# Optimization experiments

Hardware: AMD Instinct MI355X
Metric: run time of the kernel (lower is better)

The kernel has to match this reference:

```python
import jax, jax.numpy as jnp
import numpy as np

K = 11  # masked conv3d kernel size

def mask_A(k):
    # mask type 'A': flattened (i,j,t) positions with current_id < k^3//2 + 1
    # (current_id starts at 1) -> first k^3//2 positions are 1.
    m = (np.arange(k ** 3) < (k ** 3) // 2).astype(np.float32).reshape(k, k, k)
    return jnp.asarray(m)

def conv3d(x, w, b, pad):
    out = jax.lax.conv_general_dilated(
        x, w, window_strides=(1, 1, 1), padding=[(pad, pad)] * 3,
        dimension_numbers=('NCDHW', 'OIDHW', 'NCDHW'))
    return out + b[None, :, None, None, None]

def conv2d(x, w, b, pad):
    out = jax.lax.conv_general_dilated(
        x, w, window_strides=(1, 1), padding=[(pad, pad)] * 2,
        dimension_numbers=('NCHW', 'OIHW', 'NCHW'))
    return out + b[None, :, None, None]

def pconv(x, w, b):
    # 1x1x1 conv3d as channel GEMM; w: [O, C]
    return jnp.einsum('bcdhw,oc->bodhw', x, w) + b[None, :, None, None, None]

def _phi(z):
    return 0.5 * (1.0 + jax.lax.erf(z / jnp.sqrt(2.0).astype(z.dtype)))

def setup_inputs() -> dict:
    key = jax.random.key(0)
    ks = jax.random.split(key, 12)
    M = 192
    B, H, W = 1, 48, 48
    s = 0.02
    x = jax.random.normal(ks[0], (B, M, H, W), jnp.float32)
    hyper = jax.random.normal(ks[1], (B, 2 * M, H, W), jnp.float32)
    W3 = s * jax.random.normal(ks[2], (M, 2 * M, 3, 3), jnp.float32)
    b3 = jnp.zeros((M,), jnp.float32)
    W1 = s * jax.random.normal(ks[3], (24, 1, K, K, K), jnp.float32)
    b1 = jnp.zeros((24,), jnp.float32)
    Wa = s * jax.random.normal(ks[4], (48, 25), jnp.float32)
    ba = jnp.zeros((48,), jnp.float32)
    Wb = s * jax.random.normal(ks[5], (96, 48), jnp.float32)
    bb = jnp.zeros((96,), jnp.float32)
    Wc = s * jax.random.normal(ks[6], (9, 96), jnp.float32)
    bc = jnp.zeros((9,), jnp.float32)
    return {"x": x, "hyper": hyper, "W3": W3, "b3": b3, "W1": W1, "b1": b1,
            "Wa": Wa, "ba": ba, "Wb": Wb, "bb": bb, "Wc": Wc, "bc": bc}

def reference(x, hyper, W3, b3, W1, b1, Wa, ba, Wb, bb, Wc, bc):
    # x: [B,M,H,W], hyper: [B,2M,H,W]
    x5 = x[:, None]                                   # [B,1,M,H,W]
    h = conv2d(hyper, W3, b3, 1)[:, None]             # [B,1,M,H,W]
    W1m = W1 * mask_A(K)[None, None]                  # causal mask re-applied each fwd
    x1 = conv3d(x5, W1m, b1, 5)                       # [B,24,M,H,W]
    t = jnp.concatenate([x1, h], axis=1)              # [B,25,M,H,W]
    t = jax.nn.relu(pconv(t, Wa, ba))                 # [B,48,M,H,W]
    t = jax.nn.relu(pconv(t, Wb, bb))                 # [B,96,M,H,W]
    out = pconv(t, Wc, bc)                            # [B,9,M,H,W]
    # 3-component weighted Gaussian entropy model
    mu = out[:, 0:3]
    sc = out[:, 3:6]
    sc = jnp.abs(jnp.where(sc == 0.0, 1e-9, sc))
    w = jax.nn.softmax(out[:, 6:9], axis=1)
    xe = x[:, None]                                   # [B,1,M,H,W]
    lik = jnp.abs(_phi((xe + 0.5 - mu) / sc) - _phi((xe - 0.5 - mu) / sc))
    p3 = jnp.sum(w * lik, axis=1)                     # [B,M,H,W]
    return (p3, out)
```

## Files before the change

### kernel.cpp

```cpp
#include <hip/hip_runtime.h>
#include <hip/hip_fp16.h>
#include <math.h>

#define HW    2304
#define NPOS  442368

typedef _Float16 f16x8 __attribute__((ext_vector_type(8)));
typedef __fp16   h16x2 __attribute__((ext_vector_type(2)));
typedef float    f32x4 __attribute__((ext_vector_type(4)));

__device__ __forceinline__ float phi_f(float z) {
    return 0.5f * (1.0f + erff(z * 0.70710678118654752f));
}
__device__ __forceinline__ unsigned short f2h(float v) {
    _Float16 h = (_Float16)v;
    return *reinterpret_cast<unsigned short*>(&h);
}
__device__ __forceinline__ unsigned int pk2(float a, float b) {
    return (unsigned int)f2h(a) | ((unsigned int)f2h(b) << 16);
}
__device__ __forceinline__ unsigned int pkrtz(float a, float b) {
    h16x2 h = __builtin_amdgcn_cvt_pkrtz(a, b);
    return *reinterpret_cast<unsigned int*>(&h);
}

__global__ __launch_bounds__(256) void prep_all(const float* __restrict__ hyper,
                                                const float* __restrict__ W3,
                                                const float* __restrict__ W1,
                                                const float* __restrict__ Wa,
                                                const float* __restrict__ ba,
                                                const float* __restrict__ b1,
                                                const float* __restrict__ Wb,
                                                const float* __restrict__ bb,
                                                const float* __restrict__ Wc,
                                                const float* __restrict__ xg,
                                                unsigned short* __restrict__ hyperTp,
                                                unsigned short* __restrict__ apack,
                                                unsigned short* __restrict__ pk,
                                                unsigned short* __restrict__ xhp) {
    const int bx = blockIdx.x;
    if (bx < 948) {
        __shared__ float s[32][33];
        const int pt = bx % 79, it = bx / 79;
        const int tid = threadIdx.x;
        const int c = tid & 31, r = tid >> 5;
        const int pp = pt * 32 + c;
        const int yp = pp / 50, xp = pp % 50;
        const bool inter = (pp < 2500) && yp >= 1 && yp <= 48 && xp >= 1 && xp <= 48;
        const int src = inter ? ((yp - 1) * 48 + (xp - 1)) : 0;
#pragma unroll
        for (int i = 0; i < 4; ++i) {
            int icl = r + i * 8;
            s[icl][c] = inter ? hyper[(size_t)(it * 32 + icl) * HW + src] : 0.f;
        }
        __syncthreads();
#pragma unroll
        for (int i = 0; i < 4; ++i) {
            int pl = r + i * 8;
            int pp2 = pt * 32 + pl;
            if (pp2 < 2500)
                hyperTp[(size_t)pp2 * 384 + it * 32 + c] = f2h(s[c][pl]);
        }
    } else if (bx < 3540) {
        int idx = (bx - 948) * 256 + threadIdx.x;
        int j = idx & 7;
        int l = (idx >> 3) & 63;
        int rest = idx >> 9;
        int t = rest % 9; rest /= 9;
        int c = rest % 12; int T = rest / 12;
        int oc = T * 16 + (l & 15);
        int ic = c * 32 + (l >> 4) * 8 + j;
        apack[idx] = f2h(W3[((size_t)oc * 384 + ic) * 9 + t]);
    } else if (bx < 3700) {
        int idx = (bx - 3540) * 256 + threadIdx.x;
        if (idx >= 40960) return;
        float v = 0.f;
        if (idx < 31744) {
            int j = idx & 7, lane = (idx >> 3) & 63, s = (idx >> 9) & 1, c = idx >> 10;
            int q = lane >> 4;
            int oc = s * 16 + (lane & 15);
            int r = 2 * c + (q >> 1), h = q & 1, kw = 8 * h + j;
            if (oc < 24 && r < 61 && kw < 11) {
                int kd = r / 11, kh = r % 11;
                int tap = kd * 121 + kh * 11 + kw;
                if (tap < 665) v = W1[oc * 1331 + tap];
            }
        } else if (idx < 33280) {
            int i2 = idx - 31744;
            int j = i2 & 7, lane = (i2 >> 3) & 63, t = i2 >> 9;
            int m = t * 16 + (lane & 15), k = (lane >> 4) * 8 + j;
            if (k < 25) v = Wa[m * 25 + k];
            else if (k == 25) {
                float s = ba[m];
                for (int c = 0; c < 24; ++c) s += Wa[m * 25 + c] * b1[c];
                v = s;
            }
        } else if (idx < 39424) {
            int i3 = idx - 33280;
            int j = i3 & 7, lane = (i3 >> 3) & 63, k2 = (i3 >> 9) & 1, s = i3 >> 10;
            int m = s * 16 + (lane & 15), ch = k2 * 32 + (lane >> 4) * 8 + j;
            if (ch < 48) v = Wb[m * 48 + ch];
            else if (ch == 48) v = bb[m];
        } else {
            int i4 = idx - 39424;
            int j = i4 & 7, lane = (i4 >> 3) & 63, k3 = i4 >> 9;
            int m = lane & 15, ch = k3 * 32 + (lane >> 4) * 8 + j;
            if (m < 9) v = Wc[m * 96 + ch];
        }
        pk[idx] = f2h(v);
    } else {
        int idx = (bx - 3700) * 256 + threadIdx.x;
        if (idx >= 187456) return;
        int si = idx * 4;
        int zp = si / 3712, rem = si - zp * 3712;
        int yp = rem >> 6, xp0 = rem & 63;
        float f[4];
#pragma unroll
        for (int k = 0; k < 4; ++k) {
            int xp = xp0 + k;
            bool in = zp >= 5 && zp < 197 && yp >= 5 && yp < 53 && xp >= 5 && xp < 53;
            f[k] = in ? xg[(size_t)(zp - 5) * HW + (yp - 5) * 48 + (xp - 5)] : 0.f;
        }
        *(uint2*)&xhp[si] = make_uint2(pk2(f[0], f[1]), pk2(f[2], f[3]));
    }
}

__global__ __launch_bounds__(256) void conv_all(const unsigned short* __restrict__ xhp,
                                                const unsigned short* __restrict__ pk,
                                                const unsigned short* __restrict__ hyperTp,
                                                const unsigned short* __restrict__ apack,
                                                const float* __restrict__ b3,
                                                unsigned short* __restrict__ t0g,
                                                float* __restrict__ hbuf) {
    __shared__ unsigned short P[6208];
    const int tid = threadIdx.x, w = tid >> 6, lane = tid & 63;
    const int n = lane & 15, q = lane >> 4;

    if (blockIdx.x < 1728) {
        const int bx = blockIdx.x;
        const int x0 = (bx % 12) * 4, y0 = ((bx / 12) % 12) * 4, d0 = (bx / 144) * 16;

#pragma unroll
        for (int k = 0; k < 3; ++k) {
            int idx = tid + k * 256;
            if (idx < 588) {
                int row = idx >> 1, half = idx & 1;
                int py = row / 21, pz = row - py * 21;
                const uint4* src = (const uint4*)(xhp + ((size_t)(d0 + pz) * 58 + (y0 + py)) * 64
                                                  + x0 + half * 8);
                *(uint4*)&P[row * 16 + half * 8] = *src;
            }
        }
        __syncthreads();

        const f32x4 zf = {0.f, 0.f, 0.f, 0.f};
        f32x4 acc[4][2];
#pragma unroll
        for (int p = 0; p < 4; ++p) { acc[p][0] = zf; acc[p][1] = zf; }

        const f16x8* Av = (const f16x8*)pk;
        f16x8 a0 = Av[lane], a1 = Av[64 + lane];
        for (int c = 0; c < 31; ++c) {
            f16x8 ca0 = a0, ca1 = a1;
            int cn = (c < 30) ? c + 1 : 30;
            a0 = Av[cn * 128 + lane];
            a1 = Av[cn * 128 + 64 + lane];
            int r = 2 * c + (q >> 1);
            int kd = r / 11, kh = r - kd * 11;
            const unsigned short* rowp = P + ((w + kh) * 21 + (n + kd)) * 16 + (q & 1) * 8;
            unsigned int u[6];
            *(uint4*)&u[0] = *(const uint4*)(rowp);
            *(uint2*)&u[4] = *(const uint2*)(rowp + 8);
#pragma unroll
            for (int px = 0; px < 4; ++px) {
                unsigned int bw[4];
#pragma unroll
                for (int i = 0; i < 4; ++i) {
                    if ((px & 1) == 0) bw[i] = u[(px >> 1) + i];
                    else bw[i] = (u[(px >> 1) + i] >> 16) | (u[(px >> 1) + 1 + i] << 16);
                }
                f16x8 bf = *(f16x8*)bw;
                acc[px][0] = __builtin_amdgcn_mfma_f32_16x16x32_f16(ca0, bf, acc[px][0], 0, 0, 0);
                acc[px][1] = __builtin_amdgcn_mfma_f32_16x16x32_f16(ca1, bf, acc[px][1], 0, 0, 0);
            }
        }
        __syncthreads();

#pragma unroll
        for (int px = 0; px < 4; ++px) {
            unsigned int lo = pk2(acc[px][0][0], acc[px][0][1]);
            unsigned int hi = pk2(acc[px][0][2], acc[px][0][3]);
            *(uint2*)&P[(w * 16 + n) * 96 + px * 24 + q * 4] = make_uint2(lo, hi);
            if (q < 2) {
                unsigned int l2 = pk2(acc[px][1][0], acc[px][1][1]);
                unsigned int h2 = pk2(acc[px][1][2], acc[px][1][3]);
                *(uint2*)&P[(w * 16 + n) * 96 + px * 24 + 16 + q * 4] = make_uint2(l2, h2);
            }
        }
        __syncthreads();
#pragma unroll
        for (int k = 0; k < 3; ++k) {
            int idx4 = tid + k * 256;
            int row = idx4 / 12, w12 = idx4 - row * 12;
            int px = w12 / 3, third = w12 - px * 3;
            int dep = row & 15, wv = row >> 4;
            uint4 v = *(const uint4*)&P[row * 96 + px * 24 + third * 8];
            size_t pos = (size_t)(d0 + dep) * HW + (y0 + wv) * 48 + x0 + px;
            ((uint4*)t0g)[pos * 3 + third] = v;
        }
    } else {
        const int bx2 = blockIdx.x - 1728;
        const int T = bx2 % 12;
        const int g = (bx2 / 12) * 4 + w;
        const int yy = g / 3, xb = (g % 3) * 16;
        const size_t base = (size_t)(yy * 50 + xb + n) * 384 + q * 8;

        f32x4 acc = {};
        for (int c = 0; c < 12; ++c) {
            const unsigned short* ap = apack + ((size_t)(T * 12 + c) * 9) * 512 + lane * 8;
            const int coff = c * 32;
#pragma unroll
            for (int t = 0; t < 9; ++t) {
                f16x8 a = *(const f16x8*)(ap + t * 512);
                const int dd = (t / 3) * 50 + (t % 3);
                f16x8 b = *(const f16x8*)(hyperTp + base + (size_t)dd * 384 + coff);
                acc = __builtin_amdgcn_mfma_f32_16x16x32_f16(a, b, acc, 0, 0, 0);
            }
        }
#pragma unroll
        for (int e = 0; e < 4; ++e) {
            int oc = T * 16 + q * 4 + e;
            hbuf[(size_t)oc * HW + yy * 48 + xb + n] = acc[e] + b3[oc];
        }
    }
}

__global__ __launch_bounds__(128) void mlp_lik(const unsigned short* __restrict__ t0g,
                                               const float* __restrict__ hbuf,
                                               const float* __restrict__ xg,
                                               const unsigned short* __restrict__ pk,
                                               const float* __restrict__ bc,
                                               float* __restrict__ out) {
    __shared__ unsigned short t1s[2][32 * 72];
    __shared__ unsigned short t2s[2][32 * 104];
    __shared__ float oacs[2][32 * 13];
    const int tid = threadIdx.x, wv = tid >> 6, lane = tid & 63;
    const int n = lane & 15, q = lane >> 4;

    const f16x8* WaF = (const f16x8*)(pk + 31744);
    const f16x8* WbF = (const f16x8*)(pk + 33280);
    const f16x8* WcF = (const f16x8*)(pk + 39424);
    f16x8 waf[3], wbf[12], wcf[3];
#pragma unroll
    for (int s = 0; s < 3; ++s) waf[s] = WaF[s * 64 + lane];
#pragma unroll
    for (int t = 0; t < 12; ++t) wbf[t] = WbF[t * 64 + lane];
#pragma unroll
    for (int k = 0; k < 3; ++k) wcf[k] = WcF[k * 64 + lane];
    float bcv[4];
#pragma unroll
    for (int e = 0; e < 4; ++e) bcv[e] = (q * 4 + e < 9) ? bc[q * 4 + e] : 0.f;

#pragma unroll
    for (int j = 0; j < 2; ++j) {
        unsigned int lo = (q == 0) ? 0x00003C00u : 0u;
        *(uint2*)&t1s[wv][(j * 16 + n) * 72 + 48 + q * 4] = make_uint2(lo, 0u);
    }

    const f32x4 zf = {0.f, 0.f, 0.f, 0.f};
    const f16x8 z8 = {};
    const int pw0 = blockIdx.x * 256 + wv * 128;

    for (int r = 0; r < 4; ++r) {
        const int p0 = pw0 + r * 32;
        f16x8 b0[2];
#pragma unroll
        for (int j = 0; j < 2; ++j) {
            b0[j] = (q < 3) ? *(const f16x8*)(t0g + (size_t)(p0 + j * 16 + n) * 24 + q * 8)
                            : z8;
            if (q == 3) {
                float hv = hbuf[p0 + j * 16 + n];
                b0[j][0] = (_Float16)hv; b0[j][1] = (_Float16)1.0f;
            }
        }
#pragma unroll
        for (int j = 0; j < 2; ++j)
#pragma unroll
            for (int s = 0; s < 3; ++s) {
                f32x4 r1 = __builtin_amdgcn_mfma_f32_16x16x32_f16(waf[s], b0[j], zf, 0, 0, 0);
                *(uint2*)&t1s[wv][(j * 16 + n) * 72 + s * 16 + q * 4] =
                    make_uint2(pkrtz(fmaxf(r1[0], 0.f), fmaxf(r1[1], 0.f)),
                               pkrtz(fmaxf(r1[2], 0.f), fmaxf(r1[3], 0.f)));
            }
#pragma unroll
        for (int j = 0; j < 2; ++j) {
            f32x4 rb[6];
#pragma unroll
            for (int s = 0; s < 6; ++s) rb[s] = zf;
#pragma unroll
            for (int k2 = 0; k2 < 2; ++k2) {
                f16x8 bf = *(const f16x8*)&t1s[wv][(j * 16 + n) * 72 + k2 * 32 + q * 8];
#pragma unroll
                for (int s = 0; s < 6; ++s)
                    rb[s] = __builtin_amdgcn_mfma_f32_16x16x32_f16(wbf[s * 2 + k2], bf, rb[s], 0, 0, 0);
            }
#pragma unroll
            for (int s = 0; s < 6; ++s)
                *(uint2*)&t2s[wv][(j * 16 + n) * 104 + s * 16 + q * 4] =
                    make_uint2(pkrtz(fmaxf(rb[s][0], 0.f), fmaxf(rb[s][1], 0.f)),
                               pkrtz(fmaxf(rb[s][2], 0.f), fmaxf(rb[s][3], 0.f)));
        }
#pragma unroll
        for (int j = 0; j < 2; ++j) {
            f32x4 rc = zf;
#pragma unroll
            for (int k3 = 0; k3 < 3; ++k3) {
                f16x8 bf = *(const f16x8*)&t2s[wv][(j * 16 + n) * 104 + k3 * 32 + q * 8];
                rc = __builtin_amdgcn_mfma_f32_16x16x32_f16(wcf[k3], bf, rc, 0, 0, 0);
            }
#pragma unroll
            for (int e = 0; e < 4; ++e) {
                int row = q * 4 + e;
                if (row < 9) oacs[wv][(j * 16 + n) * 13 + row] = rc[e] + bcv[e];
            }
        }
        if (lane < 32) {
            float o[9];
#pragma unroll
            for (int jj = 0; jj < 9; ++jj) o[jj] = oacs[wv][lane * 13 + jj];
            const int gp = p0 + lane;
            float xv = xg[gp];
            float m = fmaxf(o[6], fmaxf(o[7], o[8]));
            float e0 = expf(o[6] - m), e1 = expf(o[7] - m), e2 = expf(o[8] - m);
            float inv_es = 1.0f / (e0 + e1 + e2);
            float p = 0.f;
#pragma unroll
            for (int jj = 0; jj < 3; ++jj) {
                float mu = o[jj];
                float sc = o[3 + jj];
                sc = (sc == 0.0f) ? 1e-9f : sc;
                sc = fabsf(sc);
                float a = phi_f((xv + 0.5f - mu) / sc);
                float b = phi_f((xv - 0.5f - mu) / sc);
                float lik = fabsf(a - b);
                float wgt = ((jj == 0) ? e0 : (jj == 1) ? e1 : e2) * inv_es;
                p = fmaf(wgt, lik, p);
            }
            out[gp] = p;
#pragma unroll
            for (int jj = 0; jj < 9; ++jj) out[NPOS + (size_t)jj * NPOS + gp] = o[jj];
        }
    }
}

extern "C" void kernel_launch(void* const* d_in, const int* in_sizes, int n_in,
                              void* d_out, int out_size, void* d_ws, size_t ws_size,
                              hipStream_t stream) {
    const float* x     = (const float*)d_in[0];
    const float* hyper = (const float*)d_in[1];
    const float* W3    = (const float*)d_in[2];
    const float* b3    = (const float*)d_in[3];
    const float* W1    = (const float*)d_in[4];
    const float* b1    = (const float*)d_in[5];
    const float* Wa    = (const float*)d_in[6];
    const float* ba    = (const float*)d_in[7];
    const float* Wb    = (const float*)d_in[8];
    const float* bb    = (const float*)d_in[9];
    const float* Wc    = (const float*)d_in[10];
    const float* bc    = (const float*)d_in[11];
    float* out = (float*)d_out;

    float* hbuf = (float*)d_ws;
    unsigned short* hyperTp = (unsigned short*)(hbuf + NPOS);
    unsigned short* apack   = hyperTp + 960000;
    unsigned short* pk      = apack + 663552;
    unsigned short* xhp     = pk + 40960;
    unsigned short* t0g     = xhp + 749824;

    prep_all<<<4433, 256, 0, stream>>>(hyper, W3, W1, Wa, ba, b1, Wb, bb, Wc, x,
                                       hyperTp, apack, pk, xhp);
    conv_all<<<2160, 256, 0, stream>>>(xhp, pk, hyperTp, apack, b3, t0g, hbuf);
    mlp_lik<<<1728, 128, 0, stream>>>(t0g, hbuf, x, pk, bc, out);
}
```

Measured before the change: 172.4 us.

## Fuse masked conv3d, hyper conv2d, and MLP/likelihood into one kernel

```diff
diff --git a/kernel.cpp b/kernel.cpp
--- a/kernel.cpp
+++ b/kernel.cpp
@@ -125,231 +125,207 @@
     }
 }
 
-__global__ __launch_bounds__(256) void conv_all(const unsigned short* __restrict__ xhp,
-                                                const unsigned short* __restrict__ pk,
-                                                const unsigned short* __restrict__ hyperTp,
-                                                const unsigned short* __restrict__ apack,
-                                                const float* __restrict__ b3,
-                                                unsigned short* __restrict__ t0g,
-                                                float* __restrict__ hbuf) {
-    __shared__ unsigned short P[6208];
+__global__ __launch_bounds__(256) void fused3(const unsigned short* __restrict__ xhp,
+                                              const unsigned short* __restrict__ pk,
+                                              const unsigned short* __restrict__ hyperTp,
+                                              const unsigned short* __restrict__ apack,
+                                              const float* __restrict__ b3,
+                                              const float* __restrict__ xg,
+                                              const float* __restrict__ bc,
+                                              float* __restrict__ out) {
+    __shared__ __align__(16) unsigned short P[6656];
+    __shared__ __align__(16) unsigned short t1s[4][1152];
+    __shared__ __align__(16) unsigned short t2s[4][1664];
+    __shared__ __align__(16) float fscr[3328];
+    __shared__ __align__(16) float htile[256];
+
     const int tid = threadIdx.x, w = tid >> 6, lane = tid & 63;
     const int n = lane & 15, q = lane >> 4;
-
-    if (blockIdx.x < 1728) {
-        const int bx = blockIdx.x;
-        const int x0 = (bx % 12) * 4, y0 = ((bx / 12) % 12) * 4, d0 = (bx / 144) * 16;
-
-#pragma unroll
-        for (int k = 0; k < 3; ++k) {
-            int idx = tid + k * 256;
-            if (idx < 588) {
-                int row = idx >> 1, half = idx & 1;
-                int py = row / 21, pz = row - py * 21;
-                const uint4* src = (const uint4*)(xhp + ((size_t)(d0 + pz) * 58 + (y0 + py)) * 64
-                                                  + x0 + half * 8);
-                *(uint4*)&P[row * 16 + half * 8] = *src;
-            }
-        }
-        __syncthreads();
-
-        const f32x4 zf = {0.f, 0.f, 0.f, 0.f};
-        f32x4 acc[4][2];
-#pragma unroll
-        for (int p = 0; p < 4; ++p) { acc[p][0] = zf; acc[p][1] = zf; }
-
-        const f16x8* Av = (const f16x8*)pk;
-        f16x8 a0 = Av[lane], a1 = Av[64 + lane];
-        for (int c = 0; c < 31; ++c) {
-            f16x8 ca0 = a0, ca1 = a1;
-            int cn = (c < 30) ? c + 1 : 30;
-            a0 = Av[cn * 128 + lane];
-            a1 = Av[cn * 128 + 64 + lane];
-            int r = 2 * c + (q >> 1);
-            int kd = r / 11, kh = r - kd * 11;
-            const unsigned short* rowp = P + ((w + kh) * 21 + (n + kd)) * 16 + (q & 1) * 8;
-            unsigned int u[6];
-            *(uint4*)&u[0] = *(const uint4*)(rowp);
-            *(uint2*)&u[4] = *(const uint2*)(rowp + 8);
-#pragma unroll
-            for (int px = 0; px < 4; ++px) {
-                unsigned int bw[4];
-#pragma unroll
-                for (int i = 0; i < 4; ++i) {
-                    if ((px & 1) == 0) bw[i] = u[(px >> 1) + i];
-                    else bw[i] = (u[(px >> 1) + i] >> 16) | (u[(px >> 1) + 1 + i] << 16);
-                }
-                f16x8 bf = *(f16x8*)bw;
-                acc[px][0] = __builtin_amdgcn_mfma_f32_16x16x32_f16(ca0, bf, acc[px][0], 0, 0, 0);
-                acc[px][1] = __builtin_amdgcn_mfma_f32_16x16x32_f16(ca1, bf, acc[px][1], 0, 0, 0);
-            }
-        }
-        __syncthreads();
-
-#pragma unroll
-        for (int px = 0; px < 4; ++px) {
-            unsigned int lo = pk2(acc[px][0][0], acc[px][0][1]);
-            unsigned int hi = pk2(acc[px][0][2], acc[px][0][3]);
-            *(uint2*)&P[(w * 16 + n) * 96 + px * 24 + q * 4] = make_uint2(lo, hi);
-            if (q < 2) {
-                unsigned int l2 = pk2(acc[px][1][0], acc[px][1][1]);
-                unsigned int h2 = pk2(acc[px][1][2], acc[px][1][3]);
-                *(uint2*)&P[(w * 16 + n) * 96 + px * 24 + 16 + q * 4] = make_uint2(l2, h2);
-            }
-        }
-        __syncthreads();
-#pragma unroll
-        for (int k = 0; k < 3; ++k) {
-            int idx4 = tid + k * 256;
-            int row = idx4 / 12, w12 = idx4 - row * 12;
-            int px = w12 / 3, third = w12 - px * 3;
-            int dep = row & 15, wv = row >> 4;
-            uint4 v = *(const uint4*)&P[row * 96 + px * 24 + third * 8];
-            size_t pos = (size_t)(d0 + dep) * HW + (y0 + wv) * 48 + x0 + px;
-            ((uint4*)t0g)[pos * 3 + third] = v;
-        }
-    } else {
-        const int bx2 = blockIdx.x - 1728;
-        const int T = bx2 % 12;
-        const int g = (bx2 / 12) * 4 + w;
-        const int yy = g / 3, xb = (g % 3) * 16;
-        const size_t base = (size_t)(yy * 50 + xb + n) * 384 + q * 8;
-
-        f32x4 acc = {};
-        for (int c = 0; c < 12; ++c) {
+    const int bx = blockIdx.x;
+    const int x0 = (bx % 12) * 4, y0 = ((bx / 12) % 12) * 4;
+    const int T = bx / 144, d0 = T * 16;
+
+#pragma unroll
+    for (int k = 0; k < 3; ++k) {
+        int idx = tid + k * 256;
+        if (idx < 588) {
+            int row = idx >> 1, half = idx & 1;
+            int py = row / 21, pz = row - py * 21;
+            const uint4* src = (const uint4*)(xhp + ((size_t)(d0 + pz) * 58 + (y0 + py)) * 64
+                                              + x0 + half * 8);
+            *(uint4*)&P[row * 16 + half * 8] = *src;
+        }
+    }
+
+    {
+        f32x4 hacc = {0.f, 0.f, 0.f, 0.f};
+        const int pp = (y0 + (n >> 2)) * 50 + x0 + (n & 3);
+        const size_t bbase = (size_t)pp * 384 + q * 8;
+        for (int cc = 0; cc < 3; ++cc) {
+            const int c = w * 3 + cc;
             const unsigned short* ap = apack + ((size_t)(T * 12 + c) * 9) * 512 + lane * 8;
             const int coff = c * 32;
 #pragma unroll
             for (int t = 0; t < 9; ++t) {
                 f16x8 a = *(const f16x8*)(ap + t * 512);
                 const int dd = (t / 3) * 50 + (t % 3);
-                f16x8 b = *(const f16x8*)(hyperTp + base + (size_t)dd * 384 + coff);
-                acc = __builtin_amdgcn_mfma_f32_16x16x32_f16(a, b, acc, 0, 0, 0);
-            }
+                f16x8 b = *(const f16x8*)(hyperTp + bbase + (size_t)dd * 384 + coff);
+                hacc = __builtin_amdgcn_mfma_f32_16x16x32_f16(a, b, hacc, 0, 0, 0);
+            }
+        }
+#pragma unroll
+        for (int e = 0; e < 4; ++e)
+            fscr[w * 256 + (q * 4 + e) * 16 + n] = hacc[e];
+    }
+    __syncthreads();
+
+    {
+        const int oc = tid >> 4, pos = tid & 15;
+        float h = b3[d0 + oc];
+#pragma unroll
+        for (int ww = 0; ww < 4; ++ww) h += fscr[ww * 256 + oc * 16 + pos];
+        htile[oc * 16 + pos] = h;
+    }
+
+    const f32x4 zf = {0.f, 0.f, 0.f, 0.f};
+    f32x4 acc[4][2];
+#pragma unroll
+    for (int p = 0; p < 4; ++p) { acc[p][0] = zf; acc[p][1] = zf; }
+
+    const f16x8* Av = (const f16x8*)pk;
+    f16x8 a0 = Av[lane], a1 = Av[64 + lane];
+    unsigned int u[6];
+    {
+        const int r0 = (q >> 1);
+        const int kd = r0 / 11, kh = r0 - kd * 11;
+        const unsigned short* rp = P + ((w + kh) * 21 + (n + kd)) * 16 + (q & 1) * 8;
+        *(uint4*)&u[0] = *(const uint4*)rp;
+        *(uint2*)&u[4] = *(const uint2*)(rp + 8);
+    }
+    for (int c = 0; c < 31; ++c) {
+        unsigned int u2[6];
+        {
+            const int r = 2 * (c + 1) + (q >> 1);
+            const int kd = r / 11, kh = r - kd * 11;
+            const unsigned short* rp = P + ((w + kh) * 21 + (n + kd)) * 16 + (q & 1) * 8;
+            *(uint4*)&u2[0] = *(const uint4*)rp;
+            *(uint2*)&u2[4] = *(const uint2*)(rp + 8);
+        }
+        f16x8 ca0 = a0, ca1 = a1;
+        const int cn = (c < 30) ? c + 1 : 30;
+        a0 = Av[cn * 128 + lane];
+        a1 = Av[cn * 128 + 64 + lane];
+#pragma unroll
+        for (int px = 0; px < 4; ++px) {
+            unsigned int bw[4];
+#pragma unroll
+            for (int i = 0; i < 4; ++i) {
+                if ((px & 1) == 0) bw[i] = u[(px >> 1) + i];
+                else bw[i] = (u[(px >> 1) + i] >> 16) | (u[(px >> 1) + 1 + i] << 16);
+            }
+            f16x8 bf = *(f16x8*)bw;
+            acc[px][0] = __builtin_amdgcn_mfma_f32_16x16x32_f16(ca0, bf, acc[px][0], 0, 0, 0);
+            acc[px][1] = __builtin_amdgcn_mfma_f32_16x16x32_f16(ca1, bf, acc[px][1], 0, 0, 0);
+        }
+#pragma unroll
+        for (int i = 0; i < 6; ++i) u[i] = u2[i];
+    }
+    __syncthreads();
+
+#pragma unroll
+    for (int px = 0; px < 4; ++px) {
+        unsigned int lo = pk2(acc[px][0][0], acc[px][0][1]);
+        unsigned int hi = pk2(acc[px][0][2], acc[px][0][3]);
+        *(uint2*)&P[(w * 16 + n) * 104 + px * 24 + q * 4] = make_uint2(lo, hi);
+        if (q < 2) {
+            unsigned int l2 = pk2(acc[px][1][0], acc[px][1][1]);
+            unsigned int h2 = pk2(acc[px][1][2], acc[px][1][3]);
+            *(uint2*)&P[(w * 16 + n) * 104 + px * 24 + 16 + q * 4] = make_uint2(l2, h2);
+        }
+    }
+
+    const volatile f16x8* WaF = (const volatile f16x8*)(pk + 31744);
+    const volatile f16x8* WbF = (const volatile f16x8*)(pk + 33280);
+    const volatile f16x8* WcF = (const volatile f16x8*)(pk + 39424);
+    float bcv[4];
+#pragma unroll
+    for (int e = 0; e < 4; ++e) bcv[e] = (q * 4 + e < 9) ? bc[q * 4 + e] : 0.f;
+    *(uint2*)&t1s[w][n * 72 + 48 + q * 4] = make_uint2((q == 0) ? 0x00003C00u : 0u, 0u);
+
+    const f16x8 z8 = {};
+    for (int px = 0; px < 4; ++px) {
+        f16x8 b0;
+        if (q < 3) {
+            b0 = *(const f16x8*)&P[(w * 16 + n) * 104 + px * 24 + q * 8];
+        } else {
+            b0 = z8;
+            b0[0] = (_Float16)htile[n * 16 + w * 4 + px];
+            b0[1] = (_Float16)1.0f;
+        }
+#pragma unroll
+        for (int s = 0; s < 3; ++s) {
+            f16x8 a = WaF[s * 64 + lane];
+            f32x4 r1 = __builtin_amdgcn_mfma_f32_16x16x32_f16(a, b0, zf, 0, 0, 0);
+            *(uint2*)&t1s[w][n * 72 + s * 16 + q * 4] =
+                make_uint2(pkrtz(fmaxf(r1[0], 0.f), fmaxf(r1[1], 0.f)),
+                           pkrtz(fmaxf(r1[2], 0.f), fmaxf(r1[3], 0.f)));
+        }
+        f32x4 rb[6];
+#pragma unroll
+        for (int s = 0; s < 6; ++s) rb[s] = zf;
+#pragma unroll
+        for (int k2 = 0; k2 < 2; ++k2) {
+            f16x8 bf = *(const f16x8*)&t1s[w][n * 72 + k2 * 32 + q * 8];
+#pragma unroll
+            for (int s = 0; s < 6; ++s) {
+                f16x8 a = WbF[(s * 2 + k2) * 64 + lane];
+                rb[s] = __builtin_amdgcn_mfma_f32_16x16x32_f16(a, bf, rb[s], 0, 0, 0);
+            }
+        }
+#pragma unroll
+        for (int s = 0; s < 6; ++s)
+            *(uint2*)&t2s[w][n * 104 + s * 16 + q * 4] =
+                make_uint2(pkrtz(fmaxf(rb[s][0], 0.f), fmaxf(rb[s][1], 0.f)),
+                           pkrtz(fmaxf(rb[s][2], 0.f), fmaxf(rb[s][3], 0.f)));
+        f32x4 rc = zf;
+#pragma unroll
+        for (int k3 = 0; k3 < 3; ++k3) {
+            f16x8 bf = *(const f16x8*)&t2s[w][n * 104 + k3 * 32 + q * 8];
+            f16x8 a = WcF[k3 * 64 + lane];
+            rc = __builtin_amdgcn_mfma_f32_16x16x32_f16(a, bf, rc, 0, 0, 0);
         }
 #pragma unroll
         for (int e = 0; e < 4; ++e) {
-            int oc = T * 16 + q * 4 + e;
-            hbuf[(size_t)oc * HW + yy * 48 + xb + n] = acc[e] + b3[oc];
-        }
-    }
-}
-
-__global__ __launch_bounds__(128) void mlp_lik(const unsigned short* __restrict__ t0g,
-                                               const float* __restrict__ hbuf,
-                                               const float* __restrict__ xg,
-                                               const unsigned short* __restrict__ pk,
-                                               const float* __restrict__ bc,
-                                               float* __restrict__ out) {
-    __shared__ unsigned short t1s[2][32 * 72];
-    __shared__ unsigned short t2s[2][32 * 104];
-    __shared__ float oacs[2][32 * 13];
-    const int tid = threadIdx.x, wv = tid >> 6, lane = tid & 63;
-    const int n = lane & 15, q = lane >> 4;
-
-    const f16x8* WaF = (const f16x8*)(pk + 31744);
-    const f16x8* WbF = (const f16x8*)(pk + 33280);
-    const f16x8* WcF = (const f16x8*)(pk + 39424);
-    f16x8 waf[3], wbf[12], wcf[3];
-#pragma unroll
-    for (int s = 0; s < 3; ++s) waf[s] = WaF[s * 64 + lane];
-#pragma unroll
-    for (int t = 0; t < 12; ++t) wbf[t] = WbF[t * 64 + lane];
-#pragma unroll
-    for (int k = 0; k < 3; ++k) wcf[k] = WcF[k * 64 + lane];
-    float bcv[4];
-#pragma unroll
-    for (int e = 0; e < 4; ++e) bcv[e] = (q * 4 + e < 9) ? bc[q * 4 + e] : 0.f;
-
-#pragma unroll
-    for (int j = 0; j < 2; ++j) {
-        unsigned int lo = (q == 0) ? 0x00003C00u : 0u;
-        *(uint2*)&t1s[wv][(j * 16 + n) * 72 + 48 + q * 4] = make_uint2(lo, 0u);
-    }
-
-    const f32x4 zf = {0.f, 0.f, 0.f, 0.f};
-    const f16x8 z8 = {};
-    const int pw0 = blockIdx.x * 256 + wv * 128;
-
-    for (int r = 0; r < 4; ++r) {
-        const int p0 = pw0 + r * 32;
-        f16x8 b0[2];
-#pragma unroll
-        for (int j = 0; j < 2; ++j) {
-            b0[j] = (q < 3) ? *(const f16x8*)(t0g + (size_t)(p0 + j * 16 + n) * 24 + q * 8)
-                            : z8;
-            if (q == 3) {
-                float hv = hbuf[p0 + j * 16 + n];
-                b0[j][0] = (_Float16)hv; b0[j][1] = (_Float16)1.0f;
-            }
-        }
-#pragma unroll
-        for (int j = 0; j < 2; ++j)
-#pragma unroll
-            for (int s = 0; s < 3; ++s) {
-                f32x4 r1 = __builtin_amdgcn_mfma_f32_16x16x32_f16(waf[s], b0[j], zf, 0, 0, 0);
-                *(uint2*)&t1s[wv][(j * 16 + n) * 72 + s * 16 + q * 4] =
-                    make_uint2(pkrtz(fmaxf(r1[0], 0.f), fmaxf(r1[1], 0.f)),
-                               pkrtz(fmaxf(r1[2], 0.f), fmaxf(r1[3], 0.f)));
-            }
-#pragma unroll
-        for (int j = 0; j < 2; ++j) {
-            f32x4 rb[6];
-#pragma unroll
-            for (int s = 0; s < 6; ++s) rb[s] = zf;
-#pragma unroll
-            for (int k2 = 0; k2 < 2; ++k2) {
-                f16x8 bf = *(const f16x8*)&t1s[wv][(j * 16 + n) * 72 + k2 * 32 + q * 8];
-#pragma unroll
-                for (int s = 0; s < 6; ++s)
-                    rb[s] = __builtin_amdgcn_mfma_f32_16x16x32_f16(wbf[s * 2 + k2], bf, rb[s], 0, 0, 0);
-            }
-#pragma unroll
-            for (int s = 0; s < 6; ++s)
-                *(uint2*)&t2s[wv][(j * 16 + n) * 104 + s * 16 + q * 4] =
-                    make_uint2(pkrtz(fmaxf(rb[s][0], 0.f), fmaxf(rb[s][1], 0.f)),
-                               pkrtz(fmaxf(rb[s][2], 0.f), fmaxf(rb[s][3], 0.f)));
-        }
-#pragma unroll
-        for (int j = 0; j < 2; ++j) {
-            f32x4 rc = zf;
-#pragma unroll
-            for (int k3 = 0; k3 < 3; ++k3) {
-                f16x8 bf = *(const f16x8*)&t2s[wv][(j * 16 + n) * 104 + k3 * 32 + q * 8];
-                rc = __builtin_amdgcn_mfma_f32_16x16x32_f16(wcf[k3], bf, rc, 0, 0, 0);
-            }
-#pragma unroll
-            for (int e = 0; e < 4; ++e) {
-                int row = q * 4 + e;
-                if (row < 9) oacs[wv][(j * 16 + n) * 13 + row] = rc[e] + bcv[e];
-            }
-        }
-        if (lane < 32) {
-            float o[9];
-#pragma unroll
-            for (int jj = 0; jj < 9; ++jj) o[jj] = oacs[wv][lane * 13 + jj];
-            const int gp = p0 + lane;
-            float xv = xg[gp];
-            float m = fmaxf(o[6], fmaxf(o[7], o[8]));
-            float e0 = expf(o[6] - m), e1 = expf(o[7] - m), e2 = expf(o[8] - m);
-            float inv_es = 1.0f / (e0 + e1 + e2);
-            float p = 0.f;
-#pragma unroll
-            for (int jj = 0; jj < 3; ++jj) {
-                float mu = o[jj];
-                float sc = o[3 + jj];
-                sc = (sc == 0.0f) ? 1e-9f : sc;
-                sc = fabsf(sc);
-                float a = phi_f((xv + 0.5f - mu) / sc);
-                float b = phi_f((xv - 0.5f - mu) / sc);
-                float lik = fabsf(a - b);
-                float wgt = ((jj == 0) ? e0 : (jj == 1) ? e1 : e2) * inv_es;
-                p = fmaf(wgt, lik, p);
-            }
-            out[gp] = p;
-#pragma unroll
-            for (int jj = 0; jj < 9; ++jj) out[NPOS + (size_t)jj * NPOS + gp] = o[jj];
-        }
+            const int row = q * 4 + e;
+            if (row < 9) fscr[w * 832 + (n * 4 + px) * 13 + row] = rc[e] + bcv[e];
+        }
+    }
+
+    {
+        float o[9];
+#pragma unroll
+        for (int jj = 0; jj < 9; ++jj) o[jj] = fscr[w * 832 + lane * 13 + jj];
+        const int gp = (d0 + (lane >> 2)) * HW + (y0 + w) * 48 + x0 + (lane & 3);
+        const float xv = xg[gp];
+        float m = fmaxf(o[6], fmaxf(o[7], o[8]));
+        float e0 = expf(o[6] - m), e1 = expf(o[7] - m), e2 = expf(o[8] - m);
+        float inv_es = 1.0f / (e0 + e1 + e2);
+        float p = 0.f;
+#pragma unroll
+        for (int jj = 0; jj < 3; ++jj) {
+            float mu = o[jj];
+            float sc = o[3 + jj];
+            sc = (sc == 0.0f) ? 1e-9f : sc;
+            sc = fabsf(sc);
+            float a = phi_f((xv + 0.5f - mu) / sc);
+            float b = phi_f((xv - 0.5f - mu) / sc);
+            float lik = fabsf(a - b);
+            float wgt = ((jj == 0) ? e0 : (jj == 1) ? e1 : e2) * inv_es;
+            p = fmaf(wgt, lik, p);
+        }
+        out[gp] = p;
+#pragma unroll
+        for (int jj = 0; jj < 9; ++jj) out[NPOS + (size_t)jj * NPOS + gp] = o[jj];
     }
 }
 
@@ -370,15 +346,12 @@
     const float* bc    = (const float*)d_in[11];
     float* out = (float*)d_out;
 
-    float* hbuf = (float*)d_ws;
-    unsigned short* hyperTp = (unsigned short*)(hbuf + NPOS);
+    unsigned short* hyperTp = (unsigned short*)d_ws;
     unsigned short* apack   = hyperTp + 960000;
     unsigned short* pk      = apack + 663552;
     unsigned short* xhp     = pk + 40960;
-    unsigned short* t0g     = xhp + 749824;
 
     prep_all<<<4433, 256, 0, stream>>>(hyper, W3, W1, Wa, ba, b1, Wb, bb, Wc, x,
                                        hyperTp, apack, pk, xhp);
-    conv_all<<<2160, 256, 0, stream>>>(xhp, pk, hyperTp, apack, b3, t0g, hbuf);
-    mlp_lik<<<1728, 128, 0, stream>>>(t0g, hbuf, x, pk, bc, out);
-}
+    fused3<<<1728, 256, 0, stream>>>(xhp, pk, hyperTp, apack, b3, x, bc, out);
+}
```

Measured after the change: 182.5 us. 1.06x slower.
